# Kernel optimization log

Hardware: AMD Instinct MI355X
Metric: run time of the kernel (lower is better)

Reference implementation:

```python
import jax, jax.numpy as jnp
import numpy as np

B, SEQ, DIM = 2, 4096, 1024
E, S = 8, 512          # num_slots = seq_len // num_experts
HID = 4 * DIM          # FeedForward hidden: dim * mult
SCALE = DIM ** 0.5     # RMSNorm scale


def rmsnorm(x, gamma):
    # matches F.normalize(x, dim=-1) * dim**0.5 * gamma (eps=1e-12 clamp on the norm)
    n = jnp.linalg.norm(x, axis=-1, keepdims=True)
    return x / jnp.maximum(n, 1e-12) * SCALE * gamma


def setup_inputs() -> dict:
    key = jax.random.key(0)
    ks = jax.random.split(key, 4)
    w_init = lambda k, shape: jax.random.normal(k, shape, dtype=jnp.float32) * 0.02
    return {
        "x": jax.random.normal(ks[0], (B, SEQ, DIM), dtype=jnp.float32),
        "norm_gamma": jnp.ones((DIM,), jnp.float32),
        "slot_norm_gamma": jnp.ones((DIM,), jnp.float32),
        "slot_embeds": jax.random.normal(ks[1], (E, S, DIM), dtype=jnp.float32),
        "w1": w_init(ks[2], (E, DIM, HID)),
        "b1": jnp.zeros((E, HID), jnp.float32),
        "w2": w_init(ks[3], (E, HID, DIM)),
        "b2": jnp.zeros((E, DIM), jnp.float32),
    }


def reference(x, norm_gamma, slot_norm_gamma, slot_embeds, w1, b1, w2, b2):
    xn = rmsnorm(x, norm_gamma)                 # [b, n, d]
    sn = rmsnorm(slot_embeds, slot_norm_gamma)  # [e, s, d]

    logits = jnp.einsum('bnd,esd->bnes', xn, sn)                   # [b, n, e, s]
    dispatch = jax.nn.softmax(logits, axis=1)                      # softmax over tokens n
    b, n, e, s = logits.shape
    combine = jax.nn.softmax(logits.reshape(b, n, e * s), axis=-1) # softmax over (e s)

    slots = jnp.einsum('bnd,bnes->besd', xn, dispatch)             # [b, e, s, d]

    # per-expert FeedForward: Linear -> GELU(exact) -> Linear (dropout=0)
    h = jnp.einsum('besd,edh->besh', slots, w1) + b1[None, :, None, :]
    h = jax.nn.gelu(h, approximate=False)
    eo = jnp.einsum('besh,ehd->besd', h, w2) + b2[None, :, None, :]

    eo = eo.reshape(b, e * s, DIM)                                 # [b, (e s), d]
    out = jnp.einsum('bmd,bnm->bnd', eo, combine)                  # [b, n, d]
    return out
```

## Files before the change

### kernel.cpp

```cpp
#include <hip/hip_runtime.h>
#include <math.h>

#define SEQ    4096
#define DIM    1024
#define NEXP   8
#define NSLOT  512
#define ES     4096
#define HID    4096
#define NB     2
#define RMS_SCALE 32.0f

typedef __attribute__((ext_vector_type(4))) float f32x4;
typedef __attribute__((ext_vector_type(8))) _Float16 f16x8;
typedef __attribute__((ext_vector_type(4))) unsigned short us4;

__device__ __forceinline__ unsigned short f2h(float f) {
    union { _Float16 h; unsigned short u; } c;
    c.h = (_Float16)f;
    return c.u;
}
__device__ __forceinline__ float h2f(unsigned short u) {
    union { unsigned short u; _Float16 h; } c;
    c.u = u;
    return (float)c.h;
}
__device__ __forceinline__ float gelu_exact(float x) {
    return 0.5f * x * (1.0f + erff(x * 0.70710678118654752f));
}

#define GLOAD_LDS16(gp, lp) \
    __builtin_amdgcn_global_load_lds((const __attribute__((address_space(1))) void*)(gp), \
                                     (__attribute__((address_space(3))) void*)(lp), 16, 0, 0)

__device__ __forceinline__ unsigned ldsoff(const void* p) {
    return (unsigned)(size_t)(const __attribute__((address_space(3))) void*)p;
}

#define DSR(dst, base, off) asm volatile("ds_read_b128 %0, %1 offset:" off : "=v"(dst) : "v"(base))
#define VM(n) asm volatile("s_waitcnt vmcnt(" #n ")" ::: "memory")
#define BAR __builtin_amdgcn_s_barrier()
#define SCB __builtin_amdgcn_sched_barrier(0)

#define PH_OPEN  BAR; asm volatile("s_waitcnt lgkmcnt(0)" ::: "memory"); SCB; \
                 __builtin_amdgcn_s_setprio(1);
#define PH_CLOSE __builtin_amdgcn_s_setprio(0);

__global__ void rmsnorm_both(const float* __restrict__ x, const float* __restrict__ ng,
                             const float* __restrict__ semb, const float* __restrict__ sg,
                             unsigned short* __restrict__ Acat, unsigned short* __restrict__ Bcat) {
    int row = blockIdx.x;
    int t = threadIdx.x;
    const bool isX = row < NB*SEQ;
    const float* in = isX ? x + (size_t)row * DIM : semb + (size_t)(row - NB*SEQ) * DIM;
    const float* gamma = isX ? ng : sg;
    unsigned short* rb = isX ? Acat + (size_t)row * 2048
                             : Bcat + (size_t)(row - NB*SEQ) * 2048;
    float4 v = reinterpret_cast<const float4*>(in)[t];
    float ss = v.x*v.x + v.y*v.y + v.z*v.z + v.w*v.w;
    #pragma unroll
    for (int off = 32; off >= 1; off >>= 1) ss += __shfl_down(ss, off, 64);
    __shared__ float red[4];
    if ((t & 63) == 0) red[t >> 6] = ss;
    __syncthreads();
    float inv = RMS_SCALE / fmaxf(sqrtf(red[0] + red[1] + red[2] + red[3]), 1e-12f);
    float4 g = reinterpret_cast<const float4*>(gamma)[t];
    float f[4] = {v.x*inv*g.x, v.y*inv*g.y, v.z*inv*g.z, v.w*inv*g.w};
    us4 hv, lv;
    #pragma unroll
    for (int q = 0; q < 4; ++q) {
        unsigned short h = f2h(f[q]);
        hv[q] = h;
        lv[q] = isX ? f2h(f[q] - h2f(h)) : h;
    }
    *reinterpret_cast<us4*>(&rb[t*4]) = hv;
    *reinterpret_cast<us4*>(&rb[1024 + t*4]) = lv;
}

__global__ void maxreduce_all(const float* __restrict__ rowpM, const float* __restrict__ colpM,
                              float* __restrict__ rmax, float* __restrict__ cmax) {
    int bx = blockIdx.x, t = threadIdx.x;
    if (bx < 32) {
        int row = bx * 256 + t;
        float m = -INFINITY;
        for (int p = 0; p < 64; ++p) m = fmaxf(m, rowpM[(size_t)p*8192 + row]);
        rmax[row] = m;
    } else {
        int fl = (bx - 32) * 256 + t;
        int b = fl >> 12, col = fl & 4095;
        float m = -INFINITY;
        for (int p = b*32; p < b*32 + 32; ++p) m = fmaxf(m, colpM[(size_t)p*4096 + col]);
        cmax[fl] = m;
    }
}

__global__ void sumreduce_all(const float* __restrict__ rowpS, const float* __restrict__ colpS,
                              float* __restrict__ rinv, float* __restrict__ cinv) {
    int bx = blockIdx.x, t = threadIdx.x;
    const float* src = (bx < 32) ? rowpS : colpS;
    float* dst = (bx < 32) ? rinv : cinv;
    int fl = (bx & 31) * 256 + t;
    float s = 0.f;
    for (int p = 0; p < 128; ++p) s += src[(size_t)p*8192 + fl];
    dst[fl] = 1.0f / s;
}

__global__ void make_weights(const float* __restrict__ logits,
                             const float* __restrict__ cmax, const float* __restrict__ rmax,
                             unsigned short* __restrict__ comb, unsigned short* __restrict__ dispT,
                             float* __restrict__ rowpS, float* __restrict__ colpS) {
    int b = blockIdx.z;
    const float* L = logits + (size_t)b * SEQ * ES;
    int n0 = blockIdx.y * 32, e0 = blockIdx.x * 32;
    int t = threadIdx.x;
    int r = t >> 3, c4 = (t & 7) * 4;
    __shared__ unsigned short tile[32][36];
    float4 v = *reinterpret_cast<const float4*>(&L[(size_t)(n0 + r) * ES + e0 + c4]);
    float rm = rmax[b*SEQ + n0 + r];
    float vv[4] = {v.x, v.y, v.z, v.w};
    us4 cb;
    float rs = 0.f;
    #pragma unroll
    for (int q = 0; q < 4; ++q) {
        cb[q] = f2h(__expf(vv[q] - rm));
        rs += h2f(cb[q]);
        float dv = __expf(vv[q] - cmax[b*ES + e0 + c4 + q]);
        tile[c4 + q][r] = f2h(dv);
    }
    *reinterpret_cast<us4*>(&comb[(size_t)b*SEQ*ES + (size_t)(n0 + r)*ES + e0 + c4]) = cb;
    rs += __shfl_xor(rs, 1, 64);
    rs += __shfl_xor(rs, 2, 64);
    rs += __shfl_xor(rs, 4, 64);
    if ((t & 7) == 0)
        rowpS[(size_t)blockIdx.x * 8192 + b*SEQ + n0 + r] = rs;
    __syncthreads();
    us4 o = *reinterpret_cast<us4*>(&tile[t >> 3][(t & 7) * 4]);
    *reinterpret_cast<us4*>(&dispT[(size_t)b*ES*SEQ + (size_t)(e0 + (t >> 3))*SEQ + n0 + (t & 7)*4]) = o;
    float cs = h2f(o[0]) + h2f(o[1]) + h2f(o[2]) + h2f(o[3]);
    cs += __shfl_xor(cs, 1, 64);
    cs += __shfl_xor(cs, 2, 64);
    cs += __shfl_xor(cs, 4, 64);
    if ((t & 7) == 0)
        colpS[(size_t)blockIdx.y * 8192 + b*ES + e0 + (t >> 3)] = cs;
}

__global__ void transpose_b16(const unsigned short* __restrict__ src, unsigned short* __restrict__ dst,
                              int sld, int dld, long sStride, long dStride) {
    int z = blockIdx.z;
    const unsigned short* S = src + (size_t)z * sStride;
    unsigned short* D = dst + (size_t)z * dStride;
    int r0 = blockIdx.y * 32, c0 = blockIdx.x * 32;
    int t = threadIdx.x;
    __shared__ unsigned short tile[32][36];
    us4 v = *reinterpret_cast<const us4*>(&S[(size_t)(r0 + (t>>3)) * sld + c0 + (t&7)*4]);
    #pragma unroll
    for (int q = 0; q < 4; ++q) tile[(t&7)*4 + q][t>>3] = v[q];
    __syncthreads();
    us4 o = *reinterpret_cast<us4*>(&tile[t >> 3][(t & 7) * 4]);
    *reinterpret_cast<us4*>(&D[(size_t)(c0 + (t>>3)) * dld + r0 + (t&7)*4]) = o;
}

__global__ void transpose_f32_h16(const float* __restrict__ src, unsigned short* __restrict__ dst,
                                  int sld, int dld, long sStride, long dStride) {
    int z = blockIdx.z;
    const float* S = src + (size_t)z * sStride;
    unsigned short* D = dst + (size_t)z * dStride;
    int r0 = blockIdx.y * 32, c0 = blockIdx.x * 32;
    int t = threadIdx.x;
    __shared__ unsigned short tile[32][36];
    float4 v = *reinterpret_cast<const float4*>(&S[(size_t)(r0 + (t>>3)) * sld + c0 + (t&7)*4]);
    float vv[4] = {v.x, v.y, v.z, v.w};
    #pragma unroll
    for (int q = 0; q < 4; ++q) tile[(t&7)*4 + q][t>>3] = f2h(vv[q]);
    __syncthreads();
    us4 o = *reinterpret_cast<us4*>(&tile[t >> 3][(t & 7) * 4]);
    *reinterpret_cast<us4*>(&D[(size_t)(c0 + (t>>3)) * dld + r0 + (t&7)*4]) = o;
}

template<int EPI, int OM, int STATS>
__global__ __launch_bounds__(512, 2)
void mfma_gemm256(const unsigned short* __restrict__ A, const unsigned short* __restrict__ B,
                  void* __restrict__ Cv, const float* __restrict__ bias,
                  int N, int K, int lda, int ldb, int ldc,
                  long aStride, long bStride, long cStride, int bMod,
                  float* __restrict__ rowpM, float* __restrict__ colpM) {
    __shared__ unsigned short lds[65536];
    const int t = threadIdx.x;
    const int lane = t & 63, wave = t >> 6;
    const int wr = wave >> 2, wc = wave & 3;
    const int z = blockIdx.z, zb = z % bMod;
    const unsigned short* Ab = A + (size_t)z * aStride;
    const unsigned short* Bb = B + (size_t)zb * bStride;
    const int gx = gridDim.x;
    int flat = blockIdx.x + blockIdx.y * gx;
    const int cpx = (gx * gridDim.y) >> 3;
    flat = (flat & 7) * cpx + (flat >> 3);
    const int m0 = (flat / gx) * 256, n0 = (flat % gx) * 256;

    const int sr = t >> 3;
    const int sg = (t & 7) ^ (sr & 7);
    const unsigned short* gA = Ab + (size_t)(m0 + sr) * lda + sg * 8;
    const unsigned short* gB = Bb + (size_t)(n0 + sr) * ldb + sg * 8;
    unsigned short* ldsw = lds + wave * 512;

    const int lr = lane & 15, lk = lane >> 4;
    const unsigned sw0 = (unsigned)(((lk)     ^ (lr & 7)) << 4);
    const unsigned sw1 = (unsigned)(((4 + lk) ^ (lr & 7)) << 4);
    const unsigned l0  = ldsoff(lds);
    const unsigned arow = (unsigned)((wr*128 + lr) * 128);
    const unsigned brow = (unsigned)((wc*64  + lr) * 128);
    const unsigned ab00 = l0 + arow + sw0,          ab10 = l0 + arow + sw1;
    const unsigned bb00 = l0 + 32768 + brow + sw0,  bb10 = l0 + 32768 + brow + sw1;
    const unsigned ab01 = ab00 + 65536, ab11 = ab10 + 65536;
    const unsigned bb01 = bb00 + 65536, bb11 = bb10 + 65536;

    #define STAGE_A(buf, half, tt) do { \
        const unsigned short* _g = gA + (size_t)((half)*128) * lda + (size_t)(tt)*64; \
        unsigned short* _l = ldsw + (buf)*32768 + (half)*8192; \
        GLOAD_LDS16(_g, _l); \
        GLOAD_LDS16(_g + (size_t)64*lda, _l + 4096); } while(0)
    #define STAGE_B(buf, half, tt) do { \
        const unsigned short* _g = gB + (size_t)((half)*128) * ldb + (size_t)(tt)*64; \
        unsigned short* _l = ldsw + (buf)*32768 + 16384 + (half)*8192; \
        GLOAD_LDS16(_g, _l); \
        GLOAD_LDS16(_g + (size_t)64*ldb, _l + 4096); } while(0)

    #define MFMA16(MB, CN) \
        _Pragma("unroll") \
        for (int m = 0; m < 4; ++m) { \
            _Pragma("unroll") \
            for (int n = 0; n < 2; ++n) { \
                acc[(MB)+m][(CN)+n] = __builtin_amdgcn_mfma_f32_16x16x32_f16(a0[m], b0[(CN)+n], acc[(MB)+m][(CN)+n], 0, 0, 0); \
                acc[(MB)+m][(CN)+n] = __builtin_amdgcn_mfma_f32_16x16x32_f16(a1[m], b1[(CN)+n], acc[(MB)+m][(CN)+n], 0, 0, 0); \
            } \
        }

    f32x4 acc[8][4] = {};
    f16x8 a0[4], a1[4], b0[4], b1[4];
    const int NT = K / 64;

    STAGE_B(0, 0, 0); STAGE_B(0, 1, 0);
    STAGE_A(0, 0, 0); STAGE_A(0, 1, 0);
    STAGE_B(1, 0, 1); STAGE_B(1, 1, 1);
    VM(4); BAR;

    for (int tt = 0; tt < NT; tt += 2) {
        const bool pf = (tt + 2 < NT);
        DSR(a0[0], ab00, "0");    DSR(a0[1], ab00, "2048");
        DSR(a0[2], ab00, "4096"); DSR(a0[3], ab00, "6144");
        DSR(a1[0], ab10, "0");    DSR(a1[1], ab10, "2048");
        DSR(a1[2], ab10, "4096"); DSR(a1[3], ab10, "6144");
        DSR(b0[0], bb00, "0");    DSR(b0[1], bb00, "2048");
        DSR(b1[0], bb10, "0");    DSR(b1[1], bb10, "2048");
        STAGE_A(1, 0, tt+1);
        PH_OPEN MFMA16(0, 0) PH_CLOSE
        BAR;
        DSR(b0[2], bb00, "4096"); DSR(b0[3], bb00, "6144");
        DSR(b1[2], bb10, "4096"); DSR(b1[3], bb10, "6144");
        STAGE_A(1, 1, tt+1);
        PH_OPEN MFMA16(0, 2) PH_CLOSE
        BAR;
        DSR(a0[0], ab00, "8192");  DSR(a0[1], ab00, "10240");
        DSR(a0[2], ab00, "12288"); DSR(a0[3], ab00, "14336");
        DSR(a1[0], ab10, "8192");  DSR(a1[1], ab10, "10240");
        DSR(a1[2], ab10, "12288"); DSR(a1[3], ab10, "14336");
        if (pf) STAGE_B(0, 0, tt+2);
        PH_OPEN MFMA16(4, 0) PH_CLOSE
        BAR;
        if (pf) STAGE_B(0, 1, tt+2);
        PH_OPEN MFMA16(4, 2) PH_CLOSE
        if (pf) { VM(4); } else { VM(0); }
        BAR;
        DSR(a0[0], ab01, "0");    DSR(a0[1], ab01, "2048");
        DSR(a0[2], ab01, "4096"); DSR(a0[3], ab01, "6144");
        DSR(a1[0], ab11, "0");    DSR(a1[1], ab11, "2048");
        DSR(a1[2], ab11, "4096"); DSR(a1[3], ab11, "6144");
        DSR(b0[0], bb01, "0");    DSR(b0[1], bb01, "2048");
        DSR(b1[0], bb11, "0");    DSR(b1[1], bb11, "2048");
        if (pf) STAGE_A(0, 0, tt+2);
        PH_OPEN MFMA16(0, 0) PH_CLOSE
        BAR;
        DSR(b0[2], bb01, "4096"); DSR(b0[3], bb01, "6144");
        DSR(b1[2], bb11, "4096"); DSR(b1[3], bb11, "6144");
        if (pf) STAGE_A(0, 1, tt+2);
        PH_OPEN MFMA16(0, 2) PH_CLOSE
        BAR;
        DSR(a0[0], ab01, "8192");  DSR(a0[1], ab01, "10240");
        DSR(a0[2], ab01, "12288"); DSR(a0[3], ab01, "14336");
        DSR(a1[0], ab11, "8192");  DSR(a1[1], ab11, "10240");
        DSR(a1[2], ab11, "12288"); DSR(a1[3], ab11, "14336");
        if (pf) STAGE_B(1, 0, tt+3);
        PH_OPEN MFMA16(4, 0) PH_CLOSE
        BAR;
        if (pf) STAGE_B(1, 1, tt+3);
        PH_OPEN MFMA16(4, 2) PH_CLOSE
        if (pf) { VM(4); } else { VM(0); }
        BAR;
    }

    if (STATS) {
        #pragma unroll
        for (int f = 0; f < 8; ++f) {
            #pragma unroll
            for (int r = 0; r < 4; ++r) {
                float m = fmaxf(fmaxf(acc[f][0][r], acc[f][1][r]), fmaxf(acc[f][2][r], acc[f][3][r]));
                #pragma unroll
                for (int msk = 1; msk <= 8; msk <<= 1) m = fmaxf(m, __shfl_xor(m, msk, 64));
                if ((lane & 15) == 0) {
                    int row = m0 + wr*128 + f*16 + (lane>>4)*4 + r;
                    int slot = (n0 >> 6) + wc;
                    rowpM[(size_t)slot*8192 + row] = m;
                }
            }
        }
        #pragma unroll
        for (int n = 0; n < 4; ++n) {
            float m = -INFINITY;
            #pragma unroll
            for (int f = 0; f < 8; ++f)
                #pragma unroll
                for (int r = 0; r < 4; ++r) m = fmaxf(m, acc[f][n][r]);
            m = fmaxf(m, __shfl_xor(m, 16, 64));
            m = fmaxf(m, __shfl_xor(m, 32, 64));
            if ((lane >> 4) == 0) {
                int col = n0 + wc*64 + n*16 + lane;
                int slot = (m0 >> 7) + wr;
                colpM[(size_t)slot*4096 + col] = m;
            }
        }
    }

    const float* bz = (EPI != 0) ? bias + (size_t)zb * N : nullptr;
    long coff = (long)z * cStride;
    int rbase = (lane >> 4) * 4;
    int cbase = lane & 15;
    #pragma unroll
    for (int f = 0; f < 8; ++f) {
        #pragma unroll
        for (int n = 0; n < 4; ++n) {
            int col  = n0 + wc*64 + n*16 + cbase;
            int row0 = m0 + wr*128 + f*16 + rbase;
            float bv = (EPI != 0) ? bz[col] : 0.f;
            float vals[4];
            #pragma unroll
            for (int r = 0; r < 4; ++r) {
                float v = acc[f][n][r] + bv;
                if (EPI == 2) v = gelu_exact(v);
                vals[r] = v;
            }
            if (OM == 0) {
                float* C = (float*)Cv + coff;
                #pragma unroll
                for (int r = 0; r < 4; ++r) C[(size_t)(row0 + r) * ldc + col] = vals[r];
            } else {
                unsigned short* C = (unsigned short*)Cv + coff;
                #pragma unroll
                for (int r = 0; r < 4; ++r) C[(size_t)(row0 + r) * ldc + col] = f2h(vals[r]);
            }
        }
    }
    #undef STAGE_A
    #undef STAGE_B
    #undef MFMA16
}

template<int EPI, int OM, int SC>
__global__ __launch_bounds__(512, 2)
void mfma_gemmX(const unsigned short* __restrict__ A, const unsigned short* __restrict__ B,
                void* __restrict__ Cv, const float* __restrict__ bias,
                int N, int K, int lda, int ldb, int ldc,
                long aStride, long bStride, long cStride, long cStrideE, int bMod,
                const float* __restrict__ svec) {
    __shared__ unsigned short lds[49152];
    const int t = threadIdx.x;
    const int lane = t & 63, wave = t >> 6;
    const int wr = wave >> 2, wc = wave & 3;
    const int z = blockIdx.z, zb = z % bMod;
    const unsigned short* Ab = A + (size_t)z * aStride;
    const unsigned short* Bb = B + (size_t)zb * bStride;
    const int gx = gridDim.x;
    int flat = blockIdx.x + blockIdx.y * gx;
    const int cpx = (gx * gridDim.y) >> 3;
    flat = (flat & 7) * cpx + (flat >> 3);
    const int m0 = (flat / gx) * 256, n0 = (flat % gx) * 128;

    const int sr = t >> 3;
    const int sg = (t & 7) ^ (sr & 7);
    const unsigned short* gA = Ab + (size_t)(m0 + sr) * lda + sg * 8;
    const unsigned short* gB = Bb + (size_t)(n0 + sr) * ldb + sg * 8;
    unsigned short* ldsw = lds + wave * 512;

    const int lr = lane & 15, lk = lane >> 4;
    const unsigned g0 = (unsigned)(((lk)     ^ (lr & 7)) << 4);
    const unsigned g1 = (unsigned)(((4 + lk) ^ (lr & 7)) << 4);
    const unsigned l0 = ldsoff(lds);
    const unsigned arow = (unsigned)((wr*64 + lr) * 128);
    const unsigned brow = (unsigned)((wc*32 + lr) * 128);
    const unsigned ax00 = l0 + arow + g0,          ax10 = l0 + arow + g1;
    const unsigned bx00 = l0 + 32768 + brow + g0,  bx10 = l0 + 32768 + brow + g1;
    const unsigned ax01 = ax00 + 49152, ax11 = ax10 + 49152;
    const unsigned bx01 = bx00 + 49152, bx11 = bx10 + 49152;

    #define STAGE_AX(buf, quad, tt) do { \
        const unsigned short* _g = gA + (size_t)((quad)*64) * lda + (size_t)(tt)*64; \
        unsigned short* _l = ldsw + (buf)*24576 + (quad)*8192; \
        GLOAD_LDS16(_g, _l); \
        GLOAD_LDS16(_g + (size_t)128*lda, _l + 4096); } while(0)
    #define STAGE_BX(buf, tt) do { \
        const unsigned short* _g = gB + (size_t)(tt)*64; \
        unsigned short* _l = ldsw + (buf)*24576 + 16384; \
        GLOAD_LDS16(_g, _l); \
        GLOAD_LDS16(_g + (size_t)64*ldb, _l + 4096); } while(0)

    #define MFMA8(MB, AR, BR) \
        _Pragma("unroll") \
        for (int m = 0; m < 4; ++m) { \
            _Pragma("unroll") \
            for (int n = 0; n < 2; ++n) { \
                acc[(MB)+m][n] = __builtin_amdgcn_mfma_f32_16x16x32_f16(AR[m], BR[n], acc[(MB)+m][n], 0, 0, 0); \
            } \
        }

    f32x4 acc[8][2] = {};
    f16x8 a0[4], a1[4], b0[2], b1[2];
    const int NT = K / 64;

    STAGE_AX(0, 0, 0); STAGE_BX(0, 0); STAGE_AX(0, 1, 0);
    STAGE_AX(1, 0, 1); STAGE_BX(1, 1);
    VM(0); BAR;

    for (int tt = 0; tt < NT; tt += 2) {
        const bool pf2 = (tt + 2 < NT);
        const bool pf3 = (tt + 3 < NT);
        DSR(a0[0], ax00, "0");    DSR(a0[1], ax00, "2048");
        DSR(a0[2], ax00, "4096"); DSR(a0[3], ax00, "6144");
        DSR(b0[0], bx00, "0");    DSR(b0[1], bx00, "2048");
        STAGE_AX(1, 1, tt+1);
        PH_OPEN MFMA8(0, a0, b0) PH_CLOSE
        BAR;
        DSR(a1[0], ax10, "0");    DSR(a1[1], ax10, "2048");
        DSR(a1[2], ax10, "4096"); DSR(a1[3], ax10, "6144");
        DSR(b1[0], bx10, "0");    DSR(b1[1], bx10, "2048");
        PH_OPEN MFMA8(0, a1, b1) PH_CLOSE
        BAR;
        DSR(a0[0], ax00, "16384"); DSR(a0[1], ax00, "18432");
        DSR(a0[2], ax00, "20480"); DSR(a0[3], ax00, "22528");
        if (pf2) STAGE_AX(0, 0, tt+2);
        PH_OPEN MFMA8(4, a0, b0) PH_CLOSE
        BAR;
        DSR(a1[0], ax10, "16384"); DSR(a1[1], ax10, "18432");
        DSR(a1[2], ax10, "20480"); DSR(a1[3], ax10, "22528");
        if (pf2) STAGE_BX(0, tt+2);
        PH_OPEN MFMA8(4, a1, b1) PH_CLOSE
        if (pf2) { VM(4); } else { VM(0); }
        BAR;
        DSR(a0[0], ax01, "0");    DSR(a0[1], ax01, "2048");
        DSR(a0[2], ax01, "4096"); DSR(a0[3], ax01, "6144");
        DSR(b0[0], bx01, "0");    DSR(b0[1], bx01, "2048");
        if (pf2) STAGE_AX(0, 1, tt+2);
        PH_OPEN MFMA8(0, a0, b0) PH_CLOSE
        BAR;
        DSR(a1[0], ax11, "0");    DSR(a1[1], ax11, "2048");
        DSR(a1[2], ax11, "4096"); DSR(a1[3], ax11, "6144");
        DSR(b1[0], bx11, "0");    DSR(b1[1], bx11, "2048");
        PH_OPEN MFMA8(0, a1, b1) PH_CLOSE
        BAR;
        DSR(a0[0], ax01, "16384"); DSR(a0[1], ax01, "18432");
        DSR(a0[2], ax01, "20480"); DSR(a0[3], ax01, "22528");
        if (pf3) STAGE_AX(1, 0, tt+3);
        PH_OPEN MFMA8(4, a0, b0) PH_CLOSE
        BAR;
        DSR(a1[0], ax11, "16384"); DSR(a1[1], ax11, "18432");
        DSR(a1[2], ax11, "20480"); DSR(a1[3], ax11, "22528");
        if (pf3) STAGE_BX(1, tt+3);
        PH_OPEN MFMA8(4, a1, b1) PH_CLOSE
        if (pf3) { VM(4); } else { VM(0); }
        BAR;
    }

    const float* bz = (EPI != 0) ? bias + (size_t)zb * N : nullptr;
    const float* sv = SC ? svec + (size_t)z * 4096 : nullptr;
    long coff = (long)z * cStride + (long)zb * cStrideE;
    int rbase = (lane >> 4) * 4;
    int cbase = lane & 15;
    #pragma unroll
    for (int f = 0; f < 8; ++f) {
        #pragma unroll
        for (int n = 0; n < 2; ++n) {
            int col  = n0 + wc*32 + n*16 + cbase;
            int row0 = m0 + wr*128 + f*16 + rbase;
            float bv = (EPI != 0) ? bz[col] : 0.f;
            float vals[4];
            #pragma unroll
            for (int r = 0; r < 4; ++r) {
                float v = acc[f][n][r] + bv;
                if (SC) v *= sv[row0 + r];
                if (EPI == 2) v = gelu_exact(v);
                vals[r] = v;
            }
            if (OM == 0) {
                float* C = (float*)Cv + coff;
                #pragma unroll
                for (int r = 0; r < 4; ++r) C[(size_t)(row0 + r) * ldc + col] = vals[r];
            } else if (OM == 1) {
                unsigned short* C = (unsigned short*)Cv + coff;
                #pragma unroll
                for (int r = 0; r < 4; ++r) C[(size_t)(row0 + r) * ldc + col] = f2h(vals[r]);
            } else {
                unsigned short* C = (unsigned short*)Cv + coff;
                us4 o;
                #pragma unroll
                for (int r = 0; r < 4; ++r) o[r] = f2h(vals[r]);
                *reinterpret_cast<us4*>(&C[(size_t)col * ldc + row0]) = o;
            }
        }
    }
    #undef STAGE_AX
    #undef STAGE_BX
    #undef MFMA8
}

extern "C" void kernel_launch(void* const* d_in, const int* in_sizes, int n_in,
                              void* d_out, int out_size, void* d_ws, size_t ws_size,
                              hipStream_t stream) {
    const float* x    = (const float*)d_in[0];
    const float* ng   = (const float*)d_in[1];
    const float* sg   = (const float*)d_in[2];
    const float* semb = (const float*)d_in[3];
    const float* w1   = (const float*)d_in[4];
    const float* b1   = (const float*)d_in[5];
    const float* w2   = (const float*)d_in[6];
    const float* b2   = (const float*)d_in[7];
    float* out = (float*)d_out;

    char* base = (char*)d_ws;
    unsigned short* Acat  = (unsigned short*)(base);
    unsigned short* Bcat  = (unsigned short*)(base + 33554432);
    unsigned short* dispT = (unsigned short*)(base);
    unsigned short* w2T   = (unsigned short*)(base);
    float*          logits= (float*)(base + 75497472);
    unsigned short* hbuf  = (unsigned short*)(base + 75497472);
    unsigned short* w1T   = (unsigned short*)(base + 142606336);
    unsigned short* xnT   = (unsigned short*)(base + 209715200);
    unsigned short* comb  = (unsigned short*)(base + 226492416);
    unsigned short* slots = (unsigned short*)(base + 293601280);
    unsigned short* eoT   = (unsigned short*)(base + 293601280);
    float* rowpM = (float*)(base + 226492416);
    float* colpM = rowpM + 64*8192;
    float* rmax  = (float*)(base + 310378496);
    float* rinv  = rmax + 8192;
    float* cmax  = rinv + 8192;
    float* cinv  = cmax + 8192;
    float* rowpS = cinv + 8192;
    float* colpS = rowpS + 128*8192;

    rmsnorm_both<<<NB*SEQ + NEXP*NSLOT, 256, 0, stream>>>(x, ng, semb, sg, Acat, Bcat);

    transpose_b16<<<dim3(DIM/32, SEQ/32, NB), 256, 0, stream>>>(
        Acat, xnT, 2048, SEQ, (long)SEQ*2048, (long)DIM*SEQ);

    mfma_gemm256<0,0,1><<<dim3(ES/256, (NB*SEQ)/256, 1), 512, 0, stream>>>(
        Acat, Bcat, logits, nullptr, ES, 2048, 2048, 2048, ES,
        0L, 0L, 0L, 1, rowpM, colpM);

    maxreduce_all<<<64, 256, 0, stream>>>(rowpM, colpM, rmax, cmax);

    make_weights<<<dim3(ES/32, SEQ/32, NB), 256, 0, stream>>>(
        logits, cmax, rmax, comb, dispT, rowpS, colpS);

    sumreduce_all<<<64, 256, 0, stream>>>(rowpS, colpS, rinv, cinv);

    transpose_f32_h16<<<dim3(HID/32, DIM/32, NEXP), 256, 0, stream>>>(
        w1, w1T, HID, DIM, (long)DIM*HID, (long)HID*DIM);

    mfma_gemmX<0,1,1><<<dim3(DIM/128, ES/256, NB), 512, 0, stream>>>(
        dispT, xnT, slots, nullptr, DIM, SEQ, SEQ, SEQ, DIM,
        (long)ES*SEQ, (long)DIM*SEQ, (long)ES*DIM, 0L, NB, cinv);

    transpose_f32_h16<<<dim3(DIM/32, HID/32, NEXP), 256, 0, stream>>>(
        w2, w2T, DIM, HID, (long)HID*DIM, (long)DIM*HID);

    mfma_gemm256<2,1,0><<<dim3(HID/256, NSLOT/256, NB*NEXP), 512, 0, stream>>>(
        slots, w1T, hbuf, b1, HID, DIM, DIM, DIM, HID,
        (long)NSLOT*DIM, (long)HID*DIM, (long)NSLOT*HID, NEXP,
        nullptr, nullptr);

    mfma_gemmX<1,2,0><<<dim3(DIM/128, NSLOT/256, NB*NEXP), 512, 0, stream>>>(
        hbuf, w2T, eoT, b2, DIM, HID, HID, HID, ES,
        (long)NSLOT*HID, (long)DIM*HID, (long)(DIM*ES/NEXP), (long)(NSLOT - DIM*ES/NEXP), NEXP,
        nullptr);

    mfma_gemmX<0,0,1><<<dim3(DIM/128, SEQ/256, NB), 512, 0, stream>>>(
        comb, eoT, out, nullptr, DIM, ES, ES, ES, DIM,
        (long)SEQ*ES, (long)DIM*ES, (long)SEQ*DIM, 0L, NB, rinv);
}
```

Before: 649.9 us.

## Merge GEMM K sub-phases to halve barriers and regroup global prefetch

Restructures the GEMM main loop so each phase loads both K-halves of A and B fragments and issues 16 MFMAs before one barrier, cutting barriers per iteration from eight to four. Global-to-LDS prefetch stages are regrouped and the vmcnt waits adjusted to match. This aims to reduce synchronization stalls and expose more MFMA back-to-back issue, at the cost of higher register pressure and possibly less latency hiding for the LDS-load waits.

```diff
diff --git a/kernel.cpp b/kernel.cpp
--- a/kernel.cpp
+++ b/kernel.cpp
@@ -411,12 +411,13 @@
         GLOAD_LDS16(_g, _l); \
         GLOAD_LDS16(_g + (size_t)64*ldb, _l + 4096); } while(0)
 
-    #define MFMA8(MB, AR, BR) \
+    #define MFMA16X(MB) \
         _Pragma("unroll") \
         for (int m = 0; m < 4; ++m) { \
             _Pragma("unroll") \
             for (int n = 0; n < 2; ++n) { \
-                acc[(MB)+m][n] = __builtin_amdgcn_mfma_f32_16x16x32_f16(AR[m], BR[n], acc[(MB)+m][n], 0, 0, 0); \
+                acc[(MB)+m][n] = __builtin_amdgcn_mfma_f32_16x16x32_f16(a0[m], b0[n], acc[(MB)+m][n], 0, 0, 0); \
+                acc[(MB)+m][n] = __builtin_amdgcn_mfma_f32_16x16x32_f16(a1[m], b1[n], acc[(MB)+m][n], 0, 0, 0); \
             } \
         }
 
@@ -429,51 +430,41 @@
     VM(0); BAR;
 
     for (int tt = 0; tt < NT; tt += 2) {
-        const bool pf2 = (tt + 2 < NT);
-        const bool pf3 = (tt + 3 < NT);
+        const bool pf = (tt + 2 < NT);
         DSR(a0[0], ax00, "0");    DSR(a0[1], ax00, "2048");
         DSR(a0[2], ax00, "4096"); DSR(a0[3], ax00, "6144");
-        DSR(b0[0], bx00, "0");    DSR(b0[1], bx00, "2048");
-        STAGE_AX(1, 1, tt+1);
-        PH_OPEN MFMA8(0, a0, b0) PH_CLOSE
-        BAR;
         DSR(a1[0], ax10, "0");    DSR(a1[1], ax10, "2048");
         DSR(a1[2], ax10, "4096"); DSR(a1[3], ax10, "6144");
+        DSR(b0[0], bx00, "0");    DSR(b0[1], bx00, "2048");
         DSR(b1[0], bx10, "0");    DSR(b1[1], bx10, "2048");
-        PH_OPEN MFMA8(0, a1, b1) PH_CLOSE
-        BAR;
+        STAGE_AX(1, 1, tt+1);
+        PH_OPEN MFMA16X(0) PH_CLOSE
+        VM(6); BAR;
         DSR(a0[0], ax00, "16384"); DSR(a0[1], ax00, "18432");
         DSR(a0[2], ax00, "20480"); DSR(a0[3], ax00, "22528");
-        if (pf2) STAGE_AX(0, 0, tt+2);
-        PH_OPEN MFMA8(4, a0, b0) PH_CLOSE
-        BAR;
         DSR(a1[0], ax10, "16384"); DSR(a1[1], ax10, "18432");
         DSR(a1[2], ax10, "20480"); DSR(a1[3], ax10, "22528");
-        if (pf2) STAGE_BX(0, tt+2);
-        PH_OPEN MFMA8(4, a1, b1) PH_CLOSE
-        if (pf2) { VM(4); } else { VM(0); }
+        if (pf) { STAGE_AX(0, 0, tt+2); STAGE_BX(0, tt+2); }
+        PH_OPEN MFMA16X(4) PH_CLOSE
+        if (pf) { VM(6); } else { VM(2); }
         BAR;
         DSR(a0[0], ax01, "0");    DSR(a0[1], ax01, "2048");
         DSR(a0[2], ax01, "4096"); DSR(a0[3], ax01, "6144");
-        DSR(b0[0], bx01, "0");    DSR(b0[1], bx01, "2048");
-        if (pf2) STAGE_AX(0, 1, tt+2);
-        PH_OPEN MFMA8(0, a0, b0) PH_CLOSE
-        BAR;
         DSR(a1[0], ax11, "0");    DSR(a1[1], ax11, "2048");
         DSR(a1[2], ax11, "4096"); DSR(a1[3], ax11, "6144");
+        DSR(b0[0], bx01, "0");    DSR(b0[1], bx01, "2048");
         DSR(b1[0], bx11, "0");    DSR(b1[1], bx11, "2048");
-        PH_OPEN MFMA8(0, a1, b1) PH_CLOSE
+        if (pf) STAGE_AX(0, 1, tt+2);
+        PH_OPEN MFMA16X(0) PH_CLOSE
+        if (pf) { VM(6); } else { VM(0); }
         BAR;
         DSR(a0[0], ax01, "16384"); DSR(a0[1], ax01, "18432");
         DSR(a0[2], ax01, "20480"); DSR(a0[3], ax01, "22528");
-        if (pf3) STAGE_AX(1, 0, tt+3);
-        PH_OPEN MFMA8(4, a0, b0) PH_CLOSE
-        BAR;
         DSR(a1[0], ax11, "16384"); DSR(a1[1], ax11, "18432");
         DSR(a1[2], ax11, "20480"); DSR(a1[3], ax11, "22528");
-        if (pf3) STAGE_BX(1, tt+3);
-        PH_OPEN MFMA8(4, a1, b1) PH_CLOSE
-        if (pf3) { VM(4); } else { VM(0); }
+        if (pf) { STAGE_AX(1, 0, tt+3); STAGE_BX(1, tt+3); }
+        PH_OPEN MFMA16X(4) PH_CLOSE
+        if (pf) { VM(6); } else { VM(0); }
         BAR;
     }
 
@@ -516,7 +507,7 @@
     }
     #undef STAGE_AX
     #undef STAGE_BX
-    #undef MFMA8
+    #undef MFMA16X
 }
 
 extern "C" void kernel_launch(void* const* d_in, const int* in_sizes, int n_in,
```

New measurement: 659.9 us. Within noise of the previous version (+1.5%).
